# Kernel tuning notes

Hardware: AMD Instinct MI355X
Metric: run time of the kernel (lower is better)

## Reference

```python
import jax, jax.numpy as jnp
import numpy as np

N_TOKENS = 100000
N_ARGS = 20000
N_EDGES = 320000
IN_DIM = 768
HEADS = 8
OUT_DIM = 64


def setup_inputs() -> dict:
    key = jax.random.key(0)
    k1, k2, k3, k4, k5 = jax.random.split(key, 5)
    h = jax.random.normal(k1, (N_TOKENS, IN_DIM), dtype=jnp.float32)
    W_fc = jax.random.normal(k2, (HEADS * OUT_DIM, IN_DIM), dtype=jnp.float32) * 0.05
    a_attn = jax.random.normal(k3, (2 * OUT_DIM,), dtype=jnp.float32) * 0.1
    edge_src = jax.random.randint(k4, (N_EDGES,), 0, N_TOKENS, dtype=jnp.int32)
    edge_dst = jax.random.randint(k5, (N_EDGES,), 0, N_ARGS, dtype=jnp.int32)
    return {"h": h, "W_fc": W_fc, "a_attn": a_attn,
            "edge_src": edge_src, "edge_dst": edge_dst}


def reference(h, W_fc, a_attn, edge_src, edge_dst):
    # z = fc(h) reshaped to [N_TOKENS, HEADS, OUT_DIM]
    z = (h @ W_fc.T).reshape(N_TOKENS, HEADS, OUT_DIM)
    # DGL zero-initializes 'z' on arg (dst) nodes, so the dst half of attn_fc
    # contributes 0; only the src half of the attention vector matters.
    a_src = a_attn[:OUT_DIM]
    s_node = jnp.einsum('nhd,d->nh', z, a_src)            # [N_TOKENS, H]
    e = jax.nn.leaky_relu(s_node[edge_src])               # [E, H]
    # segment softmax over incoming edges of each arg node
    m = jax.ops.segment_max(e, edge_dst, num_segments=N_ARGS)   # [N_ARGS, H]
    ex = jnp.exp(e - m[edge_dst])                          # [E, H]
    denom = jax.ops.segment_sum(ex, edge_dst, num_segments=N_ARGS)
    denom = jnp.where(denom == 0, 1.0, denom)
    alpha = ex / denom[edge_dst]                           # [E, H]
    # weighted neighbor aggregation
    msg = alpha[:, :, None] * z[edge_src]                  # [E, H, D]
    out = jax.ops.segment_sum(msg, edge_dst, num_segments=N_ARGS)  # [N_ARGS, H, D]
    return out
```

## Files before the change

kernel.cpp:

```cpp
#include <hip/hip_runtime.h>
#include <hip/hip_bf16.h>
#include <stdint.h>

#define N_TOKENS 100000
#define N_ARGS   20000
#define N_EDGES  320000
#define IN_DIM   768
#define HEADS    8
#define OUT_DIM  64
#define ZDIM     512

typedef unsigned short u16;
typedef unsigned int   u32;
typedef __bf16 bf16x8 __attribute__((ext_vector_type(8)));
typedef float  f32x4  __attribute__((ext_vector_type(4)));

__device__ __forceinline__ u16 f2bf(float f) {
    union { float f; u32 i; } v; v.f = f;
    u32 u = v.i;
    u += 0x7fffu + ((u >> 16) & 1u);
    return (u16)(u >> 16);
}
__device__ __forceinline__ float bf2f(u16 u) {
    union { u32 i; float f; } v; v.i = ((u32)u) << 16; return v.f;
}
__device__ __forceinline__ u32 pk(float lo, float hi) {
    __hip_bfloat162 r = __float22bfloat162_rn(float2{lo, hi});
    union { __hip_bfloat162 b; u32 u; } v; v.b = r; return v.u;
}
__device__ __forceinline__ uint4 pack8(const float4 p, const float4 q) {
    uint4 w;
    w.x = pk(p.x, p.y); w.y = pk(p.z, p.w);
    w.z = pk(q.x, q.y); w.w = pk(q.z, q.w);
    return w;
}
__device__ __forceinline__ void load_lds16(const void* g, void* l) {
    __builtin_amdgcn_global_load_lds(
        (const __attribute__((address_space(1))) void*)g,
        (__attribute__((address_space(3))) void*)l, 16, 0, 0);
}

__global__ __launch_bounds__(256) void convert_w(const float* __restrict__ W,
                                                 u16* __restrict__ Wbf) {
    const int i = blockIdx.x * blockDim.x + threadIdx.x;
    if (i < ZDIM * IN_DIM / 8) {
        const float4* p = reinterpret_cast<const float4*>(W + (size_t)i * 8);
        const float4 x = p[0], y = p[1];
        reinterpret_cast<uint4*>(Wbf)[i] = pack8(x, y);
    }
}

__global__ __launch_bounds__(256) void gemm_kernel(
    const float* __restrict__ A,
    const u16*   __restrict__ Bbf,
    const float* __restrict__ a_attn,
    u16* __restrict__ z,
    float* __restrict__ s_node)
{
    __shared__ float As[128 * 32];
    __shared__ u16   Bs[128 * 32];

    const int tid  = threadIdx.x;
    const int wave = tid >> 6, lane = tid & 63;
    const int quad = lane >> 4, l16 = lane & 15;
    const int wm = wave >> 1, wn = wave & 1;

    const int bx = blockIdx.x;
    const int lb = (bx & 7) * 391 + (bx >> 3);
    const int tileN = lb & 3;
    const int tileM = lb >> 2;

    const char* srcA[4];
    void*       dstA[4];
#pragma unroll
    for (int g = 0; g < 4; g++) {
        const int idx = (wave * 4 + g) * 64 + lane;
        const int row = idx >> 3, s = idx & 7;
        const int c = s ^ (row & 7);
        int grow = tileM * 128 + row;
        if (grow >= N_TOKENS) grow = N_TOKENS - 1;
        srcA[g] = (const char*)(A + (size_t)grow * IN_DIM + c * 4);
        dstA[g] = (char*)As + (size_t)(wave * 4 + g) * 1024;
    }
    const char* srcB[2];
    void*       dstB[2];
#pragma unroll
    for (int g = 0; g < 2; g++) {
        const int idx = (wave * 2 + g) * 64 + lane;
        const int row = idx >> 2, s = idx & 3;
        const int c = s ^ ((row >> 1) & 3);
        srcB[g] = (const char*)(Bbf + (size_t)(tileN * 128 + row) * IN_DIM + c * 8);
        dstB[g] = (char*)Bs + (size_t)(wave * 2 + g) * 1024;
    }

    const float* rA0[4];
    const float* rA1[4];
    const u16*   rB[4];
#pragma unroll
    for (int i = 0; i < 4; i++) {
        int r = wm * 64 + i * 16 + l16;
        const int sl = (quad * 2) ^ (r & 7);
        rA0[i] = As + r * 32 + sl * 4;
        rA1[i] = As + r * 32 + (sl ^ 1) * 4;
        r = wn * 64 + i * 16 + l16;
        rB[i] = Bs + r * 32 + ((quad ^ ((r >> 1) & 3)) * 8);
    }

    f32x4 acc[4][4];
    const f32x4 zero4 = {0.f, 0.f, 0.f, 0.f};
#pragma unroll
    for (int i = 0; i < 4; i++)
#pragma unroll
        for (int j = 0; j < 4; j++) acc[i][j] = zero4;

    for (int kt = 0; kt < IN_DIM / 32; ++kt) {
        __syncthreads();
#pragma unroll
        for (int g = 0; g < 4; g++) load_lds16(srcA[g], dstA[g]);
#pragma unroll
        for (int g = 0; g < 2; g++) load_lds16(srcB[g], dstB[g]);
        __syncthreads();

        bf16x8 aF[4], bF[4];
#pragma unroll
        for (int i = 0; i < 4; i++) {
            const float4 lo = *reinterpret_cast<const float4*>(rA0[i]);
            const float4 hi = *reinterpret_cast<const float4*>(rA1[i]);
            union { uint4 u; bf16x8 b; } cv;
            cv.u = pack8(lo, hi);
            aF[i] = cv.b;
        }
#pragma unroll
        for (int j = 0; j < 4; j++)
            bF[j] = *reinterpret_cast<const bf16x8*>(rB[j]);
#pragma unroll
        for (int i = 0; i < 4; i++)
#pragma unroll
            for (int j = 0; j < 4; j++)
                acc[i][j] = __builtin_amdgcn_mfma_f32_16x16x32_bf16(aF[i], bF[j], acc[i][j], 0, 0, 0);

#pragma unroll
        for (int g = 0; g < 4; g++) srcA[g] += 128;
#pragma unroll
        for (int g = 0; g < 2; g++) srcB[g] += 64;
    }

    float av[4];
#pragma unroll
    for (int j = 0; j < 4; j++) av[j] = a_attn[j * 16 + l16];
    const int head = tileN * 2 + wn;
    const int colb = tileN * 128 + wn * 64;
#pragma unroll
    for (int i = 0; i < 4; i++) {
        const int rowb = tileM * 128 + wm * 64 + i * 16 + quad * 4;
#pragma unroll
        for (int r = 0; r < 4; r++) {
            const int row = rowb + r;
            const bool ok = row < N_TOKENS;
            float p = 0.0f;
#pragma unroll
            for (int j = 0; j < 4; j++) {
                const float v = acc[i][j][r];
                p += v * av[j];
                if (ok) z[(size_t)row * ZDIM + colb + j * 16 + l16] = f2bf(v);
            }
            p += __shfl_xor(p, 1);
            p += __shfl_xor(p, 2);
            p += __shfl_xor(p, 4);
            p += __shfl_xor(p, 8);
            if (ok && l16 == 0) s_node[row * HEADS + head] = p;
        }
    }
}

__global__ void zero_kernel(int* __restrict__ p, int n) {
    int i = blockIdx.x * blockDim.x + threadIdx.x;
    if (i < n) p[i] = 0;
}

__global__ void hist_kernel(const int* __restrict__ edst, int* __restrict__ counts) {
    int i = blockIdx.x * blockDim.x + threadIdx.x;
    if (i < N_EDGES) {
        int d = edst[i];
        if ((unsigned)d < (unsigned)N_ARGS) atomicAdd(&counts[d], 1);
    }
}

__global__ void scan_kernel(const int* __restrict__ counts, int* __restrict__ offsets,
                            int* __restrict__ cursor) {
    __shared__ int partial[1024];
    const int tid = threadIdx.x;
    const int C = 20;
    const int base = tid * C;
    int s = 0;
    for (int k = 0; k < C; k++) { int idx = base + k; if (idx < N_ARGS) s += counts[idx]; }
    partial[tid] = s;
    __syncthreads();
    for (int off = 1; off < 1024; off <<= 1) {
        int v = (tid >= off) ? partial[tid - off] : 0;
        __syncthreads();
        partial[tid] += v;
        __syncthreads();
    }
    int run = (tid == 0) ? 0 : partial[tid - 1];
    for (int k = 0; k < C; k++) {
        int idx = base + k;
        if (idx < N_ARGS) { offsets[idx] = run; cursor[idx] = run; run += counts[idx]; }
    }
    if (tid == 1023) offsets[N_ARGS] = run;
}

__global__ void scatter_kernel(const int* __restrict__ esrc, const int* __restrict__ edst,
                               int* __restrict__ cursor, int* __restrict__ ssrc) {
    int i = blockIdx.x * blockDim.x + threadIdx.x;
    if (i < N_EDGES) {
        int d = edst[i];
        if ((unsigned)d >= (unsigned)N_ARGS) return;
        int s = esrc[i];
        if ((unsigned)s >= (unsigned)N_TOKENS) s = 0;
        int pos = atomicAdd(&cursor[d], 1);
        ssrc[pos] = s;
    }
}

__global__ __launch_bounds__(256) void agg_kernel(
    const int* __restrict__ offsets, const int* __restrict__ sorted_src,
    const float* __restrict__ s_node, const u16* __restrict__ z,
    float* __restrict__ out)
{
    const int dst = blockIdx.x;
    const int tid = threadIdx.x;
    const int wave = tid >> 6, lane = tid & 63;
    const int start = offsets[dst];
    const int nE = offsets[dst + 1] - start;
    if (nE <= 0) {
        out[(size_t)dst * ZDIM + tid] = 0.0f;
        out[(size_t)dst * ZDIM + tid + 256] = 0.0f;
        return;
    }
    __shared__ float m8[8];
    __shared__ float inv8[8];
    __shared__ float scratch[32];
    __shared__ int   src_lds[64];
    __shared__ float alpha_lds[64 * 8];

    float lm[8];
#pragma unroll
    for (int h = 0; h < 8; h++) lm[h] = -1e30f;
    for (int j = tid; j < nE; j += 256) {
        int s = sorted_src[start + j];
        if ((unsigned)s >= (unsigned)N_TOKENS) s = 0;
#pragma unroll
        for (int h = 0; h < 8; h++) {
            float v = s_node[s * 8 + h];
            v = v > 0.0f ? v : 0.01f * v;
            lm[h] = fmaxf(lm[h], v);
        }
    }
#pragma unroll
    for (int off = 1; off < 64; off <<= 1)
#pragma unroll
        for (int h = 0; h < 8; h++) lm[h] = fmaxf(lm[h], __shfl_xor(lm[h], off));
    if (lane == 0) {
#pragma unroll
        for (int h = 0; h < 8; h++) scratch[wave * 8 + h] = lm[h];
    }
    __syncthreads();
    if (tid < 8) {
        float r = scratch[tid];
        for (int w = 1; w < 4; w++) r = fmaxf(r, scratch[w * 8 + tid]);
        m8[tid] = r;
    }
    __syncthreads();

    float ls[8];
#pragma unroll
    for (int h = 0; h < 8; h++) ls[h] = 0.0f;
    for (int j = tid; j < nE; j += 256) {
        int s = sorted_src[start + j];
        if ((unsigned)s >= (unsigned)N_TOKENS) s = 0;
#pragma unroll
        for (int h = 0; h < 8; h++) {
            float v = s_node[s * 8 + h];
            v = v > 0.0f ? v : 0.01f * v;
            ls[h] += __expf(v - m8[h]);
        }
    }
#pragma unroll
    for (int off = 1; off < 64; off <<= 1)
#pragma unroll
        for (int h = 0; h < 8; h++) ls[h] += __shfl_xor(ls[h], off);
    if (lane == 0) {
#pragma unroll
        for (int h = 0; h < 8; h++) scratch[wave * 8 + h] = ls[h];
    }
    __syncthreads();
    if (tid < 8) {
        float d = scratch[tid];
        for (int w = 1; w < 4; w++) d += scratch[w * 8 + tid];
        if (d == 0.0f) d = 1.0f;
        inv8[tid] = 1.0f / d;
    }
    __syncthreads();

    float acc0 = 0.0f, acc1 = 0.0f;
    const int h1 = tid >> 6;
    for (int c0 = 0; c0 < nE; c0 += 64) {
        const int cn = min(64, nE - c0);
        for (int j = tid; j < cn; j += 256) {
            int s = sorted_src[start + c0 + j];
            if ((unsigned)s >= (unsigned)N_TOKENS) s = 0;
            src_lds[j] = s;
        }
        __syncthreads();
        for (int idx = tid; idx < cn * 8; idx += 256) {
            const int j = idx >> 3, h = idx & 7;
            float v = s_node[src_lds[j] * 8 + h];
            v = v > 0.0f ? v : 0.01f * v;
            alpha_lds[idx] = __expf(v - m8[h]) * inv8[h];
        }
        __syncthreads();
        for (int j = 0; j < cn; j++) {
            const int row = src_lds[j];
            acc0 += alpha_lds[j * 8 + h1]     * bf2f(z[(size_t)row * ZDIM + tid]);
            acc1 += alpha_lds[j * 8 + h1 + 4] * bf2f(z[(size_t)row * ZDIM + 256 + tid]);
        }
        __syncthreads();
    }
    out[(size_t)dst * ZDIM + tid] = acc0;
    out[(size_t)dst * ZDIM + 256 + tid] = acc1;
}

extern "C" void kernel_launch(void* const* d_in, const int* in_sizes, int n_in,
                              void* d_out, int out_size, void* d_ws, size_t ws_size,
                              hipStream_t stream) {
    const float* h      = (const float*)d_in[0];
    const float* W      = (const float*)d_in[1];
    const float* a_attn = (const float*)d_in[2];
    const int* esrc     = (const int*)d_in[3];
    const int* edst     = (const int*)d_in[4];
    float* out          = (float*)d_out;

    char* ws = (char*)d_ws;
    u16*   z        = (u16*)ws;
    float* s_node   = (float*)(ws + 102400000);
    int*   counts   = (int*)(ws + 105600000);
    int*   offsets  = (int*)(ws + 105680000);
    int*   cursor   = (int*)(ws + 105760016);
    int*   ssrc     = (int*)(ws + 105840016);
    u16*   wbf      = (u16*)(ws + 107120016);

    zero_kernel<<<(N_ARGS + 255) / 256, 256, 0, stream>>>(counts, N_ARGS);
    convert_w<<<(ZDIM * IN_DIM / 8 + 255) / 256, 256, 0, stream>>>(W, wbf);
    gemm_kernel<<<782 * 4, 256, 0, stream>>>(h, wbf, a_attn, z, s_node);
    hist_kernel<<<(N_EDGES + 255) / 256, 256, 0, stream>>>(edst, counts);
    scan_kernel<<<1, 1024, 0, stream>>>(counts, offsets, cursor);
    scatter_kernel<<<(N_EDGES + 255) / 256, 256, 0, stream>>>(esrc, edst, cursor, ssrc);
    agg_kernel<<<N_ARGS, 256, 0, stream>>>(offsets, ssrc, s_node, z, out);
}
```

Before: 717.7 us.

## Double-buffer GEMM LDS tiles and make aggregation one wave per destination

The GEMM now double-buffers its A and B LDS tiles, prefetching the next K slice while MFMAs run on the current one, so there is one barrier per iteration instead of two. The aggregation kernel is rewritten to give each destination node a single wavefront instead of a 256-thread block. That wavefront computes an online softmax in one pass using vectorized s_node loads, then gathers z rows with 16-byte loads and stages indices and alphas in per-wave LDS without block barriers. In exchange, the GEMM uses twice the LDS, which may lower occupancy, and the per-wave aggregation leaves fewer threads working per destination.

```diff
diff --git a/kernel.cpp b/kernel.cpp
--- a/kernel.cpp
+++ b/kernel.cpp
@@ -57,8 +57,8 @@
     u16* __restrict__ z,
     float* __restrict__ s_node)
 {
-    __shared__ float As[128 * 32];
-    __shared__ u16   Bs[128 * 32];
+    __shared__ float As[2][128 * 32];
+    __shared__ u16   Bs[2][128 * 32];
 
     const int tid  = threadIdx.x;
     const int wave = tid >> 6, lane = tid & 63;
@@ -71,7 +71,7 @@
     const int tileM = lb >> 2;
 
     const char* srcA[4];
-    void*       dstA[4];
+    int         dA[4];
 #pragma unroll
     for (int g = 0; g < 4; g++) {
         const int idx = (wave * 4 + g) * 64 + lane;
@@ -80,30 +80,30 @@
         int grow = tileM * 128 + row;
         if (grow >= N_TOKENS) grow = N_TOKENS - 1;
         srcA[g] = (const char*)(A + (size_t)grow * IN_DIM + c * 4);
-        dstA[g] = (char*)As + (size_t)(wave * 4 + g) * 1024;
+        dA[g] = (wave * 4 + g) * 1024;
     }
     const char* srcB[2];
-    void*       dstB[2];
+    int         dB[2];
 #pragma unroll
     for (int g = 0; g < 2; g++) {
         const int idx = (wave * 2 + g) * 64 + lane;
         const int row = idx >> 2, s = idx & 3;
         const int c = s ^ ((row >> 1) & 3);
         srcB[g] = (const char*)(Bbf + (size_t)(tileN * 128 + row) * IN_DIM + c * 8);
-        dstB[g] = (char*)Bs + (size_t)(wave * 2 + g) * 1024;
-    }
-
-    const float* rA0[4];
-    const float* rA1[4];
-    const u16*   rB[4];
+        dB[g] = (wave * 2 + g) * 1024;
+    }
+
+    const char* rA0[4];
+    const char* rA1[4];
+    const char* rB[4];
 #pragma unroll
     for (int i = 0; i < 4; i++) {
         int r = wm * 64 + i * 16 + l16;
         const int sl = (quad * 2) ^ (r & 7);
-        rA0[i] = As + r * 32 + sl * 4;
-        rA1[i] = As + r * 32 + (sl ^ 1) * 4;
+        rA0[i] = (const char*)As + r * 128 + sl * 16;
+        rA1[i] = (const char*)As + r * 128 + (sl ^ 1) * 16;
         r = wn * 64 + i * 16 + l16;
-        rB[i] = Bs + r * 32 + ((quad ^ ((r >> 1) & 3)) * 8);
+        rB[i] = (const char*)Bs + r * 64 + ((quad ^ ((r >> 1) & 3)) * 16);
     }
 
     f32x4 acc[4][4];
@@ -113,36 +113,46 @@
 #pragma unroll
         for (int j = 0; j < 4; j++) acc[i][j] = zero4;
 
+#pragma unroll
+    for (int g = 0; g < 4; g++) load_lds16(srcA[g], (char*)As + dA[g]);
+#pragma unroll
+    for (int g = 0; g < 2; g++) load_lds16(srcB[g], (char*)Bs + dB[g]);
+    __syncthreads();
+
     for (int kt = 0; kt < IN_DIM / 32; ++kt) {
-        __syncthreads();
-#pragma unroll
-        for (int g = 0; g < 4; g++) load_lds16(srcA[g], dstA[g]);
-#pragma unroll
-        for (int g = 0; g < 2; g++) load_lds16(srcB[g], dstB[g]);
-        __syncthreads();
+        const int cur = kt & 1;
+        const int nxt = cur ^ 1;
+
+        if (kt < IN_DIM / 32 - 1) {
+#pragma unroll
+            for (int g = 0; g < 4; g++)
+                load_lds16(srcA[g] + (size_t)(kt + 1) * 128,
+                           (char*)As + nxt * 16384 + dA[g]);
+#pragma unroll
+            for (int g = 0; g < 2; g++)
+                load_lds16(srcB[g] + (size_t)(kt + 1) * 64,
+                           (char*)Bs + nxt * 8192 + dB[g]);
+        }
 
         bf16x8 aF[4], bF[4];
 #pragma unroll
         for (int i = 0; i < 4; i++) {
-            const float4 lo = *reinterpret_cast<const float4*>(rA0[i]);
-            const float4 hi = *reinterpret_cast<const float4*>(rA1[i]);
+            const float4 lo = *reinterpret_cast<const float4*>(rA0[i] + cur * 16384);
+            const float4 hi = *reinterpret_cast<const float4*>(rA1[i] + cur * 16384);
             union { uint4 u; bf16x8 b; } cv;
             cv.u = pack8(lo, hi);
             aF[i] = cv.b;
         }
 #pragma unroll
         for (int j = 0; j < 4; j++)
-            bF[j] = *reinterpret_cast<const bf16x8*>(rB[j]);
+            bF[j] = *reinterpret_cast<const bf16x8*>(rB[j] + cur * 8192);
 #pragma unroll
         for (int i = 0; i < 4; i++)
 #pragma unroll
             for (int j = 0; j < 4; j++)
                 acc[i][j] = __builtin_amdgcn_mfma_f32_16x16x32_bf16(aF[i], bF[j], acc[i][j], 0, 0, 0);
 
-#pragma unroll
-        for (int g = 0; g < 4; g++) srcA[g] += 128;
-#pragma unroll
-        for (int g = 0; g < 2; g++) srcB[g] += 64;
+        __syncthreads();
     }
 
     float av[4];
@@ -228,107 +238,112 @@
     const float* __restrict__ s_node, const u16* __restrict__ z,
     float* __restrict__ out)
 {
-    const int dst = blockIdx.x;
-    const int tid = threadIdx.x;
+    const int tid  = threadIdx.x;
     const int wave = tid >> 6, lane = tid & 63;
+    const int dst  = blockIdx.x * 4 + wave;
+
+    __shared__ int   src_s[4][64];
+    __shared__ float alpha_s[4][512];
+
+    if (dst >= N_ARGS) return;
+
     const int start = offsets[dst];
     const int nE = offsets[dst + 1] - start;
+    float* op = out + (size_t)dst * ZDIM + lane * 8;
     if (nE <= 0) {
-        out[(size_t)dst * ZDIM + tid] = 0.0f;
-        out[(size_t)dst * ZDIM + tid + 256] = 0.0f;
+        const f32x4 zz = {0.f, 0.f, 0.f, 0.f};
+        *reinterpret_cast<f32x4*>(op)     = zz;
+        *reinterpret_cast<f32x4*>(op + 4) = zz;
         return;
     }
-    __shared__ float m8[8];
-    __shared__ float inv8[8];
-    __shared__ float scratch[32];
-    __shared__ int   src_lds[64];
-    __shared__ float alpha_lds[64 * 8];
-
-    float lm[8];
-#pragma unroll
-    for (int h = 0; h < 8; h++) lm[h] = -1e30f;
-    for (int j = tid; j < nE; j += 256) {
-        int s = sorted_src[start + j];
-        if ((unsigned)s >= (unsigned)N_TOKENS) s = 0;
+    int*   srcw = src_s[wave];
+    float* alw  = alpha_s[wave];
+    const int hsel = lane >> 3;
+
+    float m[8], ssum[8];
+#pragma unroll
+    for (int h = 0; h < 8; h++) { m[h] = -1e30f; ssum[h] = 0.f; }
+
+    for (int c0 = 0; c0 < nE; c0 += 64) {
+        float v[8];
+        const bool act = (c0 + lane) < nE;
+        if (act) {
+            int s = sorted_src[start + c0 + lane];
+            if ((unsigned)s >= (unsigned)N_TOKENS) s = 0;
+            const float4* p = reinterpret_cast<const float4*>(s_node + (size_t)s * 8);
+            const float4 x = p[0], y = p[1];
+            v[0]=x.x; v[1]=x.y; v[2]=x.z; v[3]=x.w;
+            v[4]=y.x; v[5]=y.y; v[6]=y.z; v[7]=y.w;
+#pragma unroll
+            for (int h = 0; h < 8; h++) v[h] = v[h] > 0.f ? v[h] : 0.01f * v[h];
+        } else {
+#pragma unroll
+            for (int h = 0; h < 8; h++) v[h] = -1e30f;
+        }
+        float cm[8];
+#pragma unroll
+        for (int h = 0; h < 8; h++) cm[h] = v[h];
+#pragma unroll
+        for (int off = 1; off < 64; off <<= 1)
+#pragma unroll
+            for (int h = 0; h < 8; h++) cm[h] = fmaxf(cm[h], __shfl_xor(cm[h], off));
+        float ce[8];
 #pragma unroll
         for (int h = 0; h < 8; h++) {
-            float v = s_node[s * 8 + h];
-            v = v > 0.0f ? v : 0.01f * v;
-            lm[h] = fmaxf(lm[h], v);
-        }
-    }
-#pragma unroll
-    for (int off = 1; off < 64; off <<= 1)
-#pragma unroll
-        for (int h = 0; h < 8; h++) lm[h] = fmaxf(lm[h], __shfl_xor(lm[h], off));
-    if (lane == 0) {
-#pragma unroll
-        for (int h = 0; h < 8; h++) scratch[wave * 8 + h] = lm[h];
-    }
-    __syncthreads();
-    if (tid < 8) {
-        float r = scratch[tid];
-        for (int w = 1; w < 4; w++) r = fmaxf(r, scratch[w * 8 + tid]);
-        m8[tid] = r;
-    }
-    __syncthreads();
-
-    float ls[8];
-#pragma unroll
-    for (int h = 0; h < 8; h++) ls[h] = 0.0f;
-    for (int j = tid; j < nE; j += 256) {
-        int s = sorted_src[start + j];
-        if ((unsigned)s >= (unsigned)N_TOKENS) s = 0;
-#pragma unroll
-        for (int h = 0; h < 8; h++) {
-            float v = s_node[s * 8 + h];
-            v = v > 0.0f ? v : 0.01f * v;
-            ls[h] += __expf(v - m8[h]);
-        }
-    }
-#pragma unroll
-    for (int off = 1; off < 64; off <<= 1)
-#pragma unroll
-        for (int h = 0; h < 8; h++) ls[h] += __shfl_xor(ls[h], off);
-    if (lane == 0) {
-#pragma unroll
-        for (int h = 0; h < 8; h++) scratch[wave * 8 + h] = ls[h];
-    }
-    __syncthreads();
-    if (tid < 8) {
-        float d = scratch[tid];
-        for (int w = 1; w < 4; w++) d += scratch[w * 8 + tid];
-        if (d == 0.0f) d = 1.0f;
-        inv8[tid] = 1.0f / d;
-    }
-    __syncthreads();
-
-    float acc0 = 0.0f, acc1 = 0.0f;
-    const int h1 = tid >> 6;
+            const float mn = fmaxf(m[h], cm[h]);
+            ce[h] = act ? __expf(v[h] - mn) : 0.f;
+            ssum[h] *= __expf(m[h] - mn);
+            m[h] = mn;
+        }
+#pragma unroll
+        for (int off = 1; off < 64; off <<= 1)
+#pragma unroll
+            for (int h = 0; h < 8; h++) ce[h] += __shfl_xor(ce[h], off);
+#pragma unroll
+        for (int h = 0; h < 8; h++) ssum[h] += ce[h];
+    }
+    float inv[8];
+#pragma unroll
+    for (int h = 0; h < 8; h++) {
+        float d = ssum[h]; if (d == 0.f) d = 1.f; inv[h] = 1.f / d;
+    }
+
+    f32x4 acc0 = {0.f,0.f,0.f,0.f}, acc1 = {0.f,0.f,0.f,0.f};
     for (int c0 = 0; c0 < nE; c0 += 64) {
         const int cn = min(64, nE - c0);
-        for (int j = tid; j < cn; j += 256) {
-            int s = sorted_src[start + c0 + j];
+        if (lane < cn) {
+            int s = sorted_src[start + c0 + lane];
             if ((unsigned)s >= (unsigned)N_TOKENS) s = 0;
-            src_lds[j] = s;
-        }
-        __syncthreads();
-        for (int idx = tid; idx < cn * 8; idx += 256) {
-            const int j = idx >> 3, h = idx & 7;
-            float v = s_node[src_lds[j] * 8 + h];
-            v = v > 0.0f ? v : 0.01f * v;
-            alpha_lds[idx] = __expf(v - m8[h]) * inv8[h];
-        }
-        __syncthreads();
-        for (int j = 0; j < cn; j++) {
-            const int row = src_lds[j];
-            acc0 += alpha_lds[j * 8 + h1]     * bf2f(z[(size_t)row * ZDIM + tid]);
-            acc1 += alpha_lds[j * 8 + h1 + 4] * bf2f(z[(size_t)row * ZDIM + 256 + tid]);
-        }
-        __syncthreads();
-    }
-    out[(size_t)dst * ZDIM + tid] = acc0;
-    out[(size_t)dst * ZDIM + 256 + tid] = acc1;
+            srcw[lane] = s;
+            const float4* p = reinterpret_cast<const float4*>(s_node + (size_t)s * 8);
+            const float4 x = p[0], y = p[1];
+            float v[8];
+            v[0]=x.x; v[1]=x.y; v[2]=x.z; v[3]=x.w;
+            v[4]=y.x; v[5]=y.y; v[6]=y.z; v[7]=y.w;
+#pragma unroll
+            for (int h = 0; h < 8; h++) {
+                const float u = v[h] > 0.f ? v[h] : 0.01f * v[h];
+                alw[lane * 8 + h] = __expf(u - m[h]) * inv[h];
+            }
+        }
+        asm volatile("s_waitcnt lgkmcnt(0)" ::: "memory");
+        for (int j = 0; j < cn; ++j) {
+            const int   row = srcw[j];
+            const float a   = alw[j * 8 + hsel];
+            const uint4 zr  = *reinterpret_cast<const uint4*>(
+                                  z + (size_t)row * ZDIM + lane * 8);
+            acc0.x += a * bf2f((u16)(zr.x & 0xffffu));
+            acc0.y += a * bf2f((u16)(zr.x >> 16));
+            acc0.z += a * bf2f((u16)(zr.y & 0xffffu));
+            acc0.w += a * bf2f((u16)(zr.y >> 16));
+            acc1.x += a * bf2f((u16)(zr.z & 0xffffu));
+            acc1.y += a * bf2f((u16)(zr.z >> 16));
+            acc1.z += a * bf2f((u16)(zr.w & 0xffffu));
+            acc1.w += a * bf2f((u16)(zr.w >> 16));
+        }
+    }
+    *reinterpret_cast<f32x4*>(op)     = acc0;
+    *reinterpret_cast<f32x4*>(op + 4) = acc1;
 }
 
 extern "C" void kernel_launch(void* const* d_in, const int* in_sizes, int n_in,
@@ -356,5 +371,5 @@
     hist_kernel<<<(N_EDGES + 255) / 256, 256, 0, stream>>>(edst, counts);
     scan_kernel<<<1, 1024, 0, stream>>>(counts, offsets, cursor);
     scatter_kernel<<<(N_EDGES + 255) / 256, 256, 0, stream>>>(esrc, edst, cursor, ssrc);
-    agg_kernel<<<N_ARGS, 256, 0, stream>>>(offsets, ssrc, s_node, z, out);
-}
+    agg_kernel<<<(N_ARGS + 3) / 4, 256, 0, stream>>>(offsets, ssrc, s_node, z, out);
+}
```

After: 711.9 us. Within noise of the previous version (-0.8%).
